# Kernel tuning notes

Measured on AMD Instinct MI355X. Metric: run time of the kernel, lower is better.

## Reference

```python
import jax, jax.numpy as jnp
import numpy as np

GAMMAS = jnp.array([2.0, 1.0, 0.5, 0.25, 0.125], dtype=jnp.float32)
K_NUM = 5
SIGN = 1.0  # min_distance=False


def setup_inputs() -> dict:
    key = jax.random.key(0)
    k1, k2 = jax.random.split(key)
    Xs = jax.random.normal(k1, (2048, 512), dtype=jnp.float32)
    Xt = jax.random.normal(k2, (2048, 512), dtype=jnp.float32)
    return {"Xs": Xs, "Xt": Xt}


def _rbf_multi(X1, X2):
    # pairwise squared distances [n1, n2], then K gamma bands -> [K, n1, n2]
    d = (X1 ** 2).sum(1)[:, None] + (X2 ** 2).sum(1)[None, :] - 2.0 * (X1 @ X2.T)
    return jnp.exp(-d[None, :, :] / (2.0 * GAMMAS[:, None, None] ** 2))


def _solve_simplex_qp(Q, p):
    # min 0.5 b^T Q b + p^T b  s.t. b >= 0, sum(b) = 1  (Q PD, K=5)
    # Exact global solve by enumerating all 31 nonempty active sets (KKT).
    K = Q.shape[0]
    masks = jnp.array([[(bits >> j) & 1 for j in range(K)]
                       for bits in range(1, 2 ** K)], dtype=Q.dtype)  # [31, K]

    def solve_one(m):
        M = jnp.zeros((K + 1, K + 1), Q.dtype)
        M = M.at[:K, :K].set(m[:, None] * Q * m[None, :] + jnp.diag(1.0 - m))
        M = M.at[:K, K].set(m)
        M = M.at[K, :K].set(m)
        rhs = jnp.concatenate([-m * p, jnp.ones((1,), Q.dtype)])
        sol = jnp.linalg.solve(M, rhs)
        beta = sol[:K] * m
        obj = 0.5 * beta @ Q @ beta + p @ beta
        feas = jnp.all(beta >= -1e-7)
        return beta, jnp.where(feas, obj, jnp.inf)

    betas, objs = jax.vmap(solve_one)(masks)
    return betas[jnp.argmin(objs)]


def reference(Xs, Xt):
    n = Xs.shape[0]
    XX = _rbf_multi(Xs, Xs)
    YY = _rbf_multi(Xt, Xt)
    YX = _rbf_multi(Xt, Xs)
    XY = _rbf_multi(Xs, Xt)
    g = XX + YY - XY - YX  # [K, n, n]

    # estimate_eta_k: pairs (i, i+1), i = 0,2,4,...
    i2 = jnp.arange(0, n, 2)
    h = g[:, i2, i2 + 1]  # [K, n/2]
    eta_p_k = 2.0 * h.sum(axis=1) / n  # [K]

    # estimate_qk_vector: h_d = h(i) - h(i+2), i = 0,4,8,...
    # inner double loop adds outer(h_d,h_d) with diagonal counted twice.
    h4 = h[:, 0::2] - h[:, 1::2]  # [K, n/4]
    Q_p_k = 4.0 / n * (h4 @ h4.T + jnp.diag((h4 ** 2).sum(axis=1)))  # [K, K]

    Q = 2.0 * Q_p_k + 1e-5 * jnp.eye(K_NUM, dtype=Q_p_k.dtype)
    p = -eta_p_k
    beta = SIGN * _solve_simplex_qp(Q, p)

    eta_k = g.mean(axis=(1, 2))  # compute_mmd
    # original detaches beta before the final dot product
    return eta_k @ jax.lax.stop_gradient(beta)
```

## Files before the change

kernel.cpp:

```cpp
#include <hip/hip_runtime.h>
#include <math.h>

#define NROWS 2048
#define DIMS  512
#define KG    5

__device__ __constant__ float c_invc[KG] = {0.125f, 0.5f, 2.0f, 8.0f, 32.0f};

typedef __attribute__((ext_vector_type(4))) int i32x4;
typedef __attribute__((ext_vector_type(8))) short bf16x8;

__device__ __forceinline__ void gload_lds16(const void* g, void* l) {
    __builtin_amdgcn_global_load_lds(
        (const __attribute__((address_space(1))) unsigned int*)g,
        (__attribute__((address_space(3))) unsigned int*)l, 16, 0, 0);
}

__device__ __forceinline__ unsigned long long pack8(const float4 v0, const float4 v1, float inv) {
    const float vv[8] = {v0.x, v0.y, v0.z, v0.w, v1.x, v1.y, v1.z, v1.w};
    unsigned long long pk = 0;
#pragma unroll
    for (int e = 0; e < 8; ++e) {
        int q = (int)rintf(vv[e] * inv);
        q = q > 127 ? 127 : (q < -127 ? -127 : q);
        pk |= (unsigned long long)((unsigned)q & 0xffu) << (8 * e);
    }
    return pk;
}

__global__ void prep_kernel(const float* __restrict__ Xs, const float* __restrict__ Xt,
                            signed char* __restrict__ Xsq, signed char* __restrict__ Xtq,
                            float* __restrict__ ns, float* __restrict__ nt,
                            float* __restrict__ sa, float* __restrict__ st,
                            float* __restrict__ h) {
    const int pairI = blockIdx.x * 4 + (threadIdx.x >> 6);
    const int lane = threadIdx.x & 63;
    const int i = 2 * pairI, j = i + 1;

    const float* psi = Xs + (size_t)i * DIMS + lane * 8;
    const float* psj = Xs + (size_t)j * DIMS + lane * 8;
    const float* pti = Xt + (size_t)i * DIMS + lane * 8;
    const float* ptj = Xt + (size_t)j * DIMS + lane * 8;
    const float4 a0 = *(const float4*)psi, a1 = *(const float4*)(psi + 4);
    const float4 b0 = *(const float4*)psj, b1 = *(const float4*)(psj + 4);
    const float4 c0 = *(const float4*)pti, c1 = *(const float4*)(pti + 4);
    const float4 d0 = *(const float4*)ptj, d1 = *(const float4*)(ptj + 4);

#define DOT8(u0, u1, v0, v1) (u0.x*v0.x + u0.y*v0.y + u0.z*v0.z + u0.w*v0.w + \
                              u1.x*v1.x + u1.y*v1.y + u1.z*v1.z + u1.w*v1.w)
#define MAX8(u0, u1) fmaxf(fmaxf(fmaxf(fabsf(u0.x), fabsf(u0.y)), fmaxf(fabsf(u0.z), fabsf(u0.w))), \
                           fmaxf(fmaxf(fabsf(u1.x), fabsf(u1.y)), fmaxf(fabsf(u1.z), fabsf(u1.w))))
    float r[8];
    r[0] = DOT8(a0, a1, a0, a1);
    r[1] = DOT8(b0, b1, b0, b1);
    r[2] = DOT8(c0, c1, c0, c1);
    r[3] = DOT8(d0, d1, d0, d1);
    r[4] = DOT8(a0, a1, b0, b1);
    r[5] = DOT8(c0, c1, d0, d1);
    r[6] = DOT8(a0, a1, d0, d1);
    r[7] = DOT8(c0, c1, b0, b1);
    float mx[4] = {MAX8(a0, a1), MAX8(b0, b1), MAX8(c0, c1), MAX8(d0, d1)};
#undef DOT8
#undef MAX8

#pragma unroll
    for (int v = 0; v < 4; ++v)
        for (int off = 32; off > 0; off >>= 1) mx[v] = fmaxf(mx[v], __shfl_xor(mx[v], off, 64));

    float inv[4], scl[4];
#pragma unroll
    for (int v = 0; v < 4; ++v) {
        scl[v] = mx[v] * (1.f / 127.f);
        inv[v] = mx[v] > 0.f ? 127.f / mx[v] : 0.f;
    }

    *(unsigned long long*)(Xsq + (size_t)i * DIMS + lane * 8) = pack8(a0, a1, inv[0]);
    *(unsigned long long*)(Xsq + (size_t)j * DIMS + lane * 8) = pack8(b0, b1, inv[1]);
    *(unsigned long long*)(Xtq + (size_t)i * DIMS + lane * 8) = pack8(c0, c1, inv[2]);
    *(unsigned long long*)(Xtq + (size_t)j * DIMS + lane * 8) = pack8(d0, d1, inv[3]);

#pragma unroll
    for (int v = 0; v < 8; ++v)
        for (int off = 32; off > 0; off >>= 1) r[v] += __shfl_down(r[v], off, 64);

    if (lane == 0) {
        ns[i] = r[0]; ns[j] = r[1]; nt[i] = r[2]; nt[j] = r[3];
        sa[i] = scl[0]; sa[j] = scl[1]; st[i] = scl[2]; st[j] = scl[3];
#pragma unroll
        for (int g = 0; g < KG; ++g) {
            const float ic = c_invc[g];
            h[g * 1024 + pairI] = __expf(-(r[0] + r[1] - 2.f * r[4]) * ic)
                                + __expf(-(r[2] + r[3] - 2.f * r[5]) * ic)
                                - __expf(-(r[0] + r[3] - 2.f * r[6]) * ic)
                                - __expf(-(r[2] + r[1] - 2.f * r[7]) * ic);
        }
    }
}

__global__ __launch_bounds__(256, 2) void gram_kernel(const signed char* __restrict__ Xsq,
                                                      const signed char* __restrict__ Xtq,
                                                      const float* __restrict__ ns,
                                                      const float* __restrict__ nt,
                                                      const float* __restrict__ sa,
                                                      const float* __restrict__ st,
                                                      float* __restrict__ partial) {
    const int pair = blockIdx.z;
    const int bx = blockIdx.x, by = blockIdx.y;
    const int bidx = pair * 256 + by * 16 + bx;
    const int tid = threadIdx.x;
    if (pair < 2 && bx < by) {
        if (tid < KG) partial[bidx * 8 + tid] = 0.f;
        return;
    }

    const signed char* A = (pair == 1) ? Xtq : Xsq;
    const signed char* B = (pair == 0) ? Xsq : Xtq;
    const float* na = (pair == 1) ? nt : ns;
    const float* nb = (pair == 0) ? ns : nt;
    const float* sca = (pair == 1) ? st : sa;
    const float* scb = (pair == 0) ? sa : st;
    const int row0 = by * 128, col0 = bx * 128;

    __shared__ signed char Asm[2][128 * 64];
    __shared__ signed char Bsm[2][128 * 64];

    const int lane = tid & 63;
    const int w = tid >> 6;
    const int wr = w >> 1, wc = w & 1;

    i32x4 acc[4][4] = {};

    const int srow = lane >> 2;
    const int schunk = lane & 3;

#define STAGE(buf, kt)                                                              \
    {                                                                               \
        _Pragma("unroll")                                                           \
        for (int q = 0; q < 2; ++q) {                                               \
            const int rbase = q * 64 + w * 16;                                      \
            const int rloc = rbase + srow;                                          \
            const int csrc = (schunk ^ ((rloc >> 1) & 3)) * 16;                     \
            gload_lds16(A + (size_t)(row0 + rloc) * DIMS + (kt) + csrc,             \
                        &Asm[buf][rbase * 64]);                                     \
            gload_lds16(B + (size_t)(col0 + rloc) * DIMS + (kt) + csrc,             \
                        &Bsm[buf][rbase * 64]);                                     \
        }                                                                           \
    }

    STAGE(0, 0);
    __syncthreads();

    const int rl = lane & 15, kq = lane >> 4;
#pragma unroll
    for (int t = 0; t < 8; ++t) {
        const int cur = t & 1;
        if (t < 7) STAGE(cur ^ 1, (t + 1) * 64);

        i32x4 af[4], bv[4];
#pragma unroll
        for (int m = 0; m < 4; ++m) {
            const int ra = wr * 64 + m * 16 + rl;
            af[m] = *(const i32x4*)&Asm[cur][ra * 64 + ((kq ^ ((ra >> 1) & 3)) * 16)];
            const int rb = wc * 64 + m * 16 + rl;
            bv[m] = *(const i32x4*)&Bsm[cur][rb * 64 + ((kq ^ ((rb >> 1) & 3)) * 16)];
        }
#pragma unroll
        for (int m = 0; m < 4; ++m)
#pragma unroll
            for (int n = 0; n < 4; ++n)
                acc[m][n] = __builtin_amdgcn_mfma_i32_16x16x64_i8(af[m], bv[n], acc[m][n], 0, 0, 0);
        __syncthreads();
    }
#undef STAGE

    float lsum[KG] = {0.f, 0.f, 0.f, 0.f, 0.f};
    const int gcol0 = col0 + wc * 64 + rl;
    const int grow0 = row0 + wr * 64 + kq * 4;
    const bool diagTile = (pair < 2) && (bx == by);
    const float wgt = (pair == 2) ? 1.f : 2.f;

    float colnorm[4], colscale[4];
#pragma unroll
    for (int n = 0; n < 4; ++n) {
        colnorm[n] = nb[gcol0 + n * 16];
        colscale[n] = scb[gcol0 + n * 16];
    }

#pragma unroll
    for (int m = 0; m < 4; ++m) {
        const float4 rn4 = *(const float4*)&na[grow0 + m * 16];
        const float4 rs4 = *(const float4*)&sca[grow0 + m * 16];
        const float rn[4] = {rn4.x, rn4.y, rn4.z, rn4.w};
        const float rs[4] = {rs4.x, rs4.y, rs4.z, rs4.w};
#pragma unroll
        for (int jj = 0; jj < 4; ++jj) {
            const int grow = grow0 + m * 16 + jj;
#pragma unroll
            for (int n = 0; n < 4; ++n) {
                const int gcol = gcol0 + n * 16;
                const float d = rn[jj] + colnorm[n]
                              - 2.f * (rs[jj] * colscale[n]) * (float)acc[m][n][jj];
                if (diagTile && gcol == grow) {
#pragma unroll
                    for (int g = 0; g < KG; ++g) lsum[g] += 1.f;
                } else if ((!diagTile || gcol > grow) && d < 840.f) {
                    float e = __expf(-d * 0.125f);
#pragma unroll
                    for (int g = 0; g < KG; ++g) {
                        lsum[g] += wgt * e;
                        const float e2 = e * e;
                        e = e2 * e2;
                    }
                }
            }
        }
    }

    __shared__ float redf[KG][4];
#pragma unroll
    for (int g = 0; g < KG; ++g) {
        float v = lsum[g];
        for (int off = 32; off > 0; off >>= 1) v += __shfl_down(v, off, 64);
        if (lane == 0) redf[g][w] = v;
    }
    __syncthreads();
    if (tid < KG)
        partial[bidx * 8 + tid] = redf[tid][0] + redf[tid][1] + redf[tid][2] + redf[tid][3];
}

__global__ void finalize_kernel(const float* __restrict__ partial,
                                const float* __restrict__ h,
                                float* __restrict__ out) {
    __shared__ float h4[KG][512];
    __shared__ float hsumS[KG];
    __shared__ float qdotS[15];
    __shared__ float redh[KG][4];
    __shared__ double sumsS[16];
    const int t = threadIdx.x;
    const int wv = t >> 6, ln = t & 63;

    if (wv < 3) {
        double s[KG] = {0.0, 0.0, 0.0, 0.0, 0.0};
        for (int b = ln; b < 256; b += 64) {
            const float* p = &partial[(wv * 256 + b) * 8];
#pragma unroll
            for (int g = 0; g < KG; ++g) s[g] += (double)p[g];
        }
#pragma unroll
        for (int g = 0; g < KG; ++g) {
            double v = s[g];
            for (int off = 32; off > 0; off >>= 1) v += __shfl_down(v, off, 64);
            if (ln == 0) sumsS[wv * KG + g] = v;
        }
    }

    for (int k = 0; k < KG; ++k)
        for (int j2 = t; j2 < 512; j2 += 256)
            h4[k][j2] = h[k * 1024 + 2 * j2] - h[k * 1024 + 2 * j2 + 1];

    {
        float s[KG] = {0.f, 0.f, 0.f, 0.f, 0.f};
        for (int j = t; j < 1024; j += 256)
#pragma unroll
            for (int k = 0; k < KG; ++k) s[k] += h[k * 1024 + j];
#pragma unroll
        for (int k = 0; k < KG; ++k) {
            float v = s[k];
            for (int off = 32; off > 0; off >>= 1) v += __shfl_down(v, off, 64);
            if (ln == 0) redh[k][wv] = v;
        }
    }
    __syncthreads();
    if (t < KG) hsumS[t] = redh[t][0] + redh[t][1] + redh[t][2] + redh[t][3];
    __syncthreads();

    const int pa[15] = {0,0,0,0,0,1,1,1,1,2,2,2,3,3,4};
    const int pb[15] = {0,1,2,3,4,1,2,3,4,2,3,4,3,4,4};
    for (int pi = wv; pi < 15; pi += 4) {
        float s = 0.f;
        for (int j = ln; j < 512; j += 64) s += h4[pa[pi]][j] * h4[pb[pi]][j];
        for (int off = 32; off > 0; off >>= 1) s += __shfl_down(s, off, 64);
        if (ln == 0) qdotS[pi] = s;
    }
    __syncthreads();

    if (t < 64) {
        const double n = 2048.0;
        double Q[KG][KG], p[KG], eta[KG];
        {
            int idx = 0;
            double dd[KG][KG];
#pragma unroll
            for (int a = 0; a < KG; ++a)
#pragma unroll
                for (int b = a; b < KG; ++b) { dd[a][b] = qdotS[idx]; dd[b][a] = qdotS[idx]; ++idx; }
#pragma unroll
            for (int a = 0; a < KG; ++a)
#pragma unroll
                for (int b = 0; b < KG; ++b) {
                    double qp = (4.0 / n) * (dd[a][b] + ((a == b) ? dd[a][a] : 0.0));
                    Q[a][b] = 2.0 * qp + ((a == b) ? 1e-5 : 0.0);
                }
        }
#pragma unroll
        for (int k = 0; k < KG; ++k) {
            p[k] = -2.0 * (double)hsumS[k] / n;
            eta[k] = (sumsS[k] + sumsS[KG + k] - 2.0 * sumsS[2 * KG + k]) / (n * n);
        }

        const int mask = t;
        const bool valid = (mask >= 1 && mask < 32);
        double beta[KG] = {0, 0, 0, 0, 0};
        double obj = INFINITY;

        if (valid) {
            double m[KG];
#pragma unroll
            for (int k = 0; k < KG; ++k) m[k] = (mask >> k) & 1 ? 1.0 : 0.0;
            double M[6][7];
#pragma unroll
            for (int a = 0; a < 6; ++a)
#pragma unroll
                for (int b = 0; b < 7; ++b) M[a][b] = 0.0;
#pragma unroll
            for (int a = 0; a < KG; ++a) {
#pragma unroll
                for (int b = 0; b < KG; ++b) M[a][b] = m[a] * Q[a][b] * m[b];
                M[a][a] += 1.0 - m[a];
                M[a][KG] = m[a];
                M[KG][a] = m[a];
                M[a][6] = -m[a] * p[a];
            }
            M[KG][6] = 1.0;
#pragma unroll
            for (int col = 0; col < 6; ++col) {
                const double dinv = 1.0 / M[col][col];
#pragma unroll
                for (int rr = 0; rr < 6; ++rr) {
                    if (rr > col) {
                        const double f = M[rr][col] * dinv;
#pragma unroll
                        for (int c = 0; c < 7; ++c)
                            if (c >= col) M[rr][c] -= f * M[col][c];
                    }
                }
            }
            double sol[6];
#pragma unroll
            for (int rr = 5; rr >= 0; --rr) {
                double s = M[rr][6];
#pragma unroll
                for (int c = 0; c < 6; ++c)
                    if (c > rr) s -= M[rr][c] * sol[c];
                sol[rr] = s / M[rr][rr];
            }
#pragma unroll
            for (int k = 0; k < KG; ++k) beta[k] = sol[k] * m[k];
            double o = 0.0;
#pragma unroll
            for (int a = 0; a < KG; ++a) {
                double qb = 0.0;
#pragma unroll
                for (int b = 0; b < KG; ++b) qb += Q[a][b] * beta[b];
                o += 0.5 * beta[a] * qb + p[a] * beta[a];
            }
            bool feas = true;
#pragma unroll
            for (int k = 0; k < KG; ++k) if (!(beta[k] >= -1e-7)) feas = false;
            obj = feas ? o : INFINITY;
        }

        double bobj = obj;
        int blane = valid ? mask : 9999;
        for (int off = 32; off > 0; off >>= 1) {
            const double o2 = __shfl_down(bobj, off, 64);
            const int l2 = __shfl_down(blane, off, 64);
            if (o2 < bobj || (o2 == bobj && l2 < blane)) { bobj = o2; blane = l2; }
        }
        bobj = __shfl(bobj, 0, 64);
        blane = __shfl(blane, 0, 64);
        if (bobj > 1e300) blane = 1;

        if (mask == blane) {
            double o = 0.0;
#pragma unroll
            for (int k = 0; k < KG; ++k) o += eta[k] * beta[k];
            out[0] = (float)o;
        }
    }
}

extern "C" void kernel_launch(void* const* d_in, const int* in_sizes, int n_in,
                              void* d_out, int out_size, void* d_ws, size_t ws_size,
                              hipStream_t stream) {
    const float* Xs = (const float*)d_in[0];
    const float* Xt = (const float*)d_in[1];
    float* out = (float*)d_out;

    char* ws = (char*)d_ws;
    float* partial = (float*)ws;
    float* ns = (float*)(ws + 24576);
    float* nt = (float*)(ws + 32768);
    float* sa = (float*)(ws + 40960);
    float* st = (float*)(ws + 49152);
    float* h  = (float*)(ws + 57344);
    signed char* Xsq = (signed char*)(ws + 131072);
    signed char* Xtq = (signed char*)(ws + 131072 + 1048576);

    prep_kernel<<<256, 256, 0, stream>>>(Xs, Xt, Xsq, Xtq, ns, nt, sa, st, h);
    gram_kernel<<<dim3(16, 16, 3), 256, 0, stream>>>(Xsq, Xtq, ns, nt, sa, st, partial);
    finalize_kernel<<<1, 256, 0, stream>>>(partial, h, out);
}
```

Before: 37.09 us.

## Treat stacked Xs/Xt as one Gram matrix and compute only upper-triangle tiles

The two inputs are quantized into one stacked 4096-row matrix, and the gram kernel launches only the 528 upper-triangle 128x128 tiles. Cross blocks get weight -2 and diagonal blocks are handled symmetrically. This removes the early-exit blocks of the old 768-block grid and the separate XY pass. The K step per stage is also doubled to 128 with a wider LDS swizzle, which halves the number of barriers but doubles LDS use per block. Tile decode uses a serial while loop per block.

```diff
diff --git a/kernel.cpp b/kernel.cpp
--- a/kernel.cpp
+++ b/kernel.cpp
@@ -2,13 +2,14 @@
 #include <math.h>
 
 #define NROWS 2048
+#define ZROWS 4096
 #define DIMS  512
 #define KG    5
+#define NJOBS 528
 
 __device__ __constant__ float c_invc[KG] = {0.125f, 0.5f, 2.0f, 8.0f, 32.0f};
 
 typedef __attribute__((ext_vector_type(4))) int i32x4;
-typedef __attribute__((ext_vector_type(8))) short bf16x8;
 
 __device__ __forceinline__ void gload_lds16(const void* g, void* l) {
     __builtin_amdgcn_global_load_lds(
@@ -29,9 +30,8 @@
 }
 
 __global__ void prep_kernel(const float* __restrict__ Xs, const float* __restrict__ Xt,
-                            signed char* __restrict__ Xsq, signed char* __restrict__ Xtq,
-                            float* __restrict__ ns, float* __restrict__ nt,
-                            float* __restrict__ sa, float* __restrict__ st,
+                            signed char* __restrict__ Zq,
+                            float* __restrict__ nz, float* __restrict__ sz,
                             float* __restrict__ h) {
     const int pairI = blockIdx.x * 4 + (threadIdx.x >> 6);
     const int lane = threadIdx.x & 63;
@@ -74,18 +74,18 @@
         inv[v] = mx[v] > 0.f ? 127.f / mx[v] : 0.f;
     }
 
-    *(unsigned long long*)(Xsq + (size_t)i * DIMS + lane * 8) = pack8(a0, a1, inv[0]);
-    *(unsigned long long*)(Xsq + (size_t)j * DIMS + lane * 8) = pack8(b0, b1, inv[1]);
-    *(unsigned long long*)(Xtq + (size_t)i * DIMS + lane * 8) = pack8(c0, c1, inv[2]);
-    *(unsigned long long*)(Xtq + (size_t)j * DIMS + lane * 8) = pack8(d0, d1, inv[3]);
+    *(unsigned long long*)(Zq + (size_t)i * DIMS + lane * 8)            = pack8(a0, a1, inv[0]);
+    *(unsigned long long*)(Zq + (size_t)j * DIMS + lane * 8)            = pack8(b0, b1, inv[1]);
+    *(unsigned long long*)(Zq + (size_t)(NROWS + i) * DIMS + lane * 8)  = pack8(c0, c1, inv[2]);
+    *(unsigned long long*)(Zq + (size_t)(NROWS + j) * DIMS + lane * 8)  = pack8(d0, d1, inv[3]);
 
 #pragma unroll
     for (int v = 0; v < 8; ++v)
         for (int off = 32; off > 0; off >>= 1) r[v] += __shfl_down(r[v], off, 64);
 
     if (lane == 0) {
-        ns[i] = r[0]; ns[j] = r[1]; nt[i] = r[2]; nt[j] = r[3];
-        sa[i] = scl[0]; sa[j] = scl[1]; st[i] = scl[2]; st[j] = scl[3];
+        nz[i] = r[0]; nz[j] = r[1]; nz[NROWS + i] = r[2]; nz[NROWS + j] = r[3];
+        sz[i] = scl[0]; sz[j] = scl[1]; sz[NROWS + i] = scl[2]; sz[NROWS + j] = scl[3];
 #pragma unroll
         for (int g = 0; g < KG; ++g) {
             const float ic = c_invc[g];
@@ -97,53 +97,39 @@
     }
 }
 
-__global__ __launch_bounds__(256, 2) void gram_kernel(const signed char* __restrict__ Xsq,
-                                                      const signed char* __restrict__ Xtq,
-                                                      const float* __restrict__ ns,
-                                                      const float* __restrict__ nt,
-                                                      const float* __restrict__ sa,
-                                                      const float* __restrict__ st,
+__global__ __launch_bounds__(256, 2) void gram_kernel(const signed char* __restrict__ Zq,
+                                                      const float* __restrict__ nz,
+                                                      const float* __restrict__ sz,
                                                       float* __restrict__ partial) {
-    const int pair = blockIdx.z;
-    const int bx = blockIdx.x, by = blockIdx.y;
-    const int bidx = pair * 256 + by * 16 + bx;
+    int job = blockIdx.x;
+    int by = 0;
+    while (job >= (32 - by)) { job -= (32 - by); ++by; }
+    const int bx = by + job;
+
+    const int row0 = by * 128, col0 = bx * 128;
     const int tid = threadIdx.x;
-    if (pair < 2 && bx < by) {
-        if (tid < KG) partial[bidx * 8 + tid] = 0.f;
-        return;
-    }
-
-    const signed char* A = (pair == 1) ? Xtq : Xsq;
-    const signed char* B = (pair == 0) ? Xsq : Xtq;
-    const float* na = (pair == 1) ? nt : ns;
-    const float* nb = (pair == 0) ? ns : nt;
-    const float* sca = (pair == 1) ? st : sa;
-    const float* scb = (pair == 0) ? sa : st;
-    const int row0 = by * 128, col0 = bx * 128;
-
-    __shared__ signed char Asm[2][128 * 64];
-    __shared__ signed char Bsm[2][128 * 64];
-
     const int lane = tid & 63;
     const int w = tid >> 6;
     const int wr = w >> 1, wc = w & 1;
 
+    __shared__ signed char Asm[2][128 * 128];
+    __shared__ signed char Bsm[2][128 * 128];
+
     i32x4 acc[4][4] = {};
 
-    const int srow = lane >> 2;
-    const int schunk = lane & 3;
+    const int lrow = lane >> 3;
+    const int lchunk = (lane & 7) ^ lrow;
 
 #define STAGE(buf, kt)                                                              \
     {                                                                               \
         _Pragma("unroll")                                                           \
-        for (int q = 0; q < 2; ++q) {                                               \
-            const int rbase = q * 64 + w * 16;                                      \
-            const int rloc = rbase + srow;                                          \
-            const int csrc = (schunk ^ ((rloc >> 1) & 3)) * 16;                     \
-            gload_lds16(A + (size_t)(row0 + rloc) * DIMS + (kt) + csrc,             \
-                        &Asm[buf][rbase * 64]);                                     \
-            gload_lds16(B + (size_t)(col0 + rloc) * DIMS + (kt) + csrc,             \
-                        &Bsm[buf][rbase * 64]);                                     \
+        for (int q = 0; q < 4; ++q) {                                               \
+            const int rbase = w * 32 + q * 8;                                       \
+            const int rloc = rbase + lrow;                                          \
+            gload_lds16(Zq + (size_t)(row0 + rloc) * DIMS + (kt) + lchunk * 16,     \
+                        &Asm[buf][rbase * 128]);                                    \
+            gload_lds16(Zq + (size_t)(col0 + rloc) * DIMS + (kt) + lchunk * 16,     \
+                        &Bsm[buf][rbase * 128]);                                    \
         }                                                                           \
     }
 
@@ -152,23 +138,26 @@
 
     const int rl = lane & 15, kq = lane >> 4;
 #pragma unroll
-    for (int t = 0; t < 8; ++t) {
+    for (int t = 0; t < 4; ++t) {
         const int cur = t & 1;
-        if (t < 7) STAGE(cur ^ 1, (t + 1) * 64);
-
-        i32x4 af[4], bv[4];
-#pragma unroll
-        for (int m = 0; m < 4; ++m) {
-            const int ra = wr * 64 + m * 16 + rl;
-            af[m] = *(const i32x4*)&Asm[cur][ra * 64 + ((kq ^ ((ra >> 1) & 3)) * 16)];
-            const int rb = wc * 64 + m * 16 + rl;
-            bv[m] = *(const i32x4*)&Bsm[cur][rb * 64 + ((kq ^ ((rb >> 1) & 3)) * 16)];
-        }
-#pragma unroll
-        for (int m = 0; m < 4; ++m)
-#pragma unroll
-            for (int n = 0; n < 4; ++n)
-                acc[m][n] = __builtin_amdgcn_mfma_i32_16x16x64_i8(af[m], bv[n], acc[m][n], 0, 0, 0);
+        if (t < 3) STAGE(cur ^ 1, (t + 1) * 128);
+
+#pragma unroll
+        for (int sub = 0; sub < 2; ++sub) {
+            i32x4 af[4], bv[4];
+#pragma unroll
+            for (int m = 0; m < 4; ++m) {
+                const int ra = wr * 64 + m * 16 + rl;
+                af[m] = *(const i32x4*)&Asm[cur][ra * 128 + (((sub * 4 + kq) ^ (ra & 7)) * 16)];
+                const int rb = wc * 64 + m * 16 + rl;
+                bv[m] = *(const i32x4*)&Bsm[cur][rb * 128 + (((sub * 4 + kq) ^ (rb & 7)) * 16)];
+            }
+#pragma unroll
+            for (int m = 0; m < 4; ++m)
+#pragma unroll
+                for (int n = 0; n < 4; ++n)
+                    acc[m][n] = __builtin_amdgcn_mfma_i32_16x16x64_i8(af[m], bv[n], acc[m][n], 0, 0, 0);
+        }
         __syncthreads();
     }
 #undef STAGE
@@ -176,20 +165,21 @@
     float lsum[KG] = {0.f, 0.f, 0.f, 0.f, 0.f};
     const int gcol0 = col0 + wc * 64 + rl;
     const int grow0 = row0 + wr * 64 + kq * 4;
-    const bool diagTile = (pair < 2) && (bx == by);
-    const float wgt = (pair == 2) ? 1.f : 2.f;
+    const bool diagTile = (bx == by);
+    const bool sameQuad = ((bx < 16) == (by < 16));
+    const float wgt = sameQuad ? 2.f : -2.f;
 
     float colnorm[4], colscale[4];
 #pragma unroll
     for (int n = 0; n < 4; ++n) {
-        colnorm[n] = nb[gcol0 + n * 16];
-        colscale[n] = scb[gcol0 + n * 16];
+        colnorm[n] = nz[gcol0 + n * 16];
+        colscale[n] = sz[gcol0 + n * 16];
     }
 
 #pragma unroll
     for (int m = 0; m < 4; ++m) {
-        const float4 rn4 = *(const float4*)&na[grow0 + m * 16];
-        const float4 rs4 = *(const float4*)&sca[grow0 + m * 16];
+        const float4 rn4 = *(const float4*)&nz[grow0 + m * 16];
+        const float4 rs4 = *(const float4*)&sz[grow0 + m * 16];
         const float rn[4] = {rn4.x, rn4.y, rn4.z, rn4.w};
         const float rs[4] = {rs4.x, rs4.y, rs4.z, rs4.w};
 #pragma unroll
@@ -225,7 +215,7 @@
     }
     __syncthreads();
     if (tid < KG)
-        partial[bidx * 8 + tid] = redf[tid][0] + redf[tid][1] + redf[tid][2] + redf[tid][3];
+        partial[blockIdx.x * 8 + tid] = redf[tid][0] + redf[tid][1] + redf[tid][2] + redf[tid][3];
 }
 
 __global__ void finalize_kernel(const float* __restrict__ partial,
@@ -235,14 +225,15 @@
     __shared__ float hsumS[KG];
     __shared__ float qdotS[15];
     __shared__ float redh[KG][4];
-    __shared__ double sumsS[16];
+    __shared__ double redd[4][KG];
+    __shared__ double sumsS[KG];
     const int t = threadIdx.x;
     const int wv = t >> 6, ln = t & 63;
 
-    if (wv < 3) {
+    {
         double s[KG] = {0.0, 0.0, 0.0, 0.0, 0.0};
-        for (int b = ln; b < 256; b += 64) {
-            const float* p = &partial[(wv * 256 + b) * 8];
+        for (int b = t; b < NJOBS; b += 256) {
+            const float* p = &partial[b * 8];
 #pragma unroll
             for (int g = 0; g < KG; ++g) s[g] += (double)p[g];
         }
@@ -250,7 +241,7 @@
         for (int g = 0; g < KG; ++g) {
             double v = s[g];
             for (int off = 32; off > 0; off >>= 1) v += __shfl_down(v, off, 64);
-            if (ln == 0) sumsS[wv * KG + g] = v;
+            if (ln == 0) redd[wv][g] = v;
         }
     }
 
@@ -271,7 +262,10 @@
         }
     }
     __syncthreads();
-    if (t < KG) hsumS[t] = redh[t][0] + redh[t][1] + redh[t][2] + redh[t][3];
+    if (t < KG) {
+        hsumS[t] = redh[t][0] + redh[t][1] + redh[t][2] + redh[t][3];
+        sumsS[t] = redd[0][t] + redd[1][t] + redd[2][t] + redd[3][t];
+    }
     __syncthreads();
 
     const int pa[15] = {0,0,0,0,0,1,1,1,1,2,2,2,3,3,4};
@@ -305,7 +299,7 @@
 #pragma unroll
         for (int k = 0; k < KG; ++k) {
             p[k] = -2.0 * (double)hsumS[k] / n;
-            eta[k] = (sumsS[k] + sumsS[KG + k] - 2.0 * sumsS[2 * KG + k]) / (n * n);
+            eta[k] = sumsS[k] / (n * n);
         }
 
         const int mask = t;
@@ -399,15 +393,12 @@
 
     char* ws = (char*)d_ws;
     float* partial = (float*)ws;
-    float* ns = (float*)(ws + 24576);
-    float* nt = (float*)(ws + 32768);
-    float* sa = (float*)(ws + 40960);
-    float* st = (float*)(ws + 49152);
-    float* h  = (float*)(ws + 57344);
-    signed char* Xsq = (signed char*)(ws + 131072);
-    signed char* Xtq = (signed char*)(ws + 131072 + 1048576);
-
-    prep_kernel<<<256, 256, 0, stream>>>(Xs, Xt, Xsq, Xtq, ns, nt, sa, st, h);
-    gram_kernel<<<dim3(16, 16, 3), 256, 0, stream>>>(Xsq, Xtq, ns, nt, sa, st, partial);
+    float* nz = (float*)(ws + 32768);
+    float* sz = (float*)(ws + 32768 + 16384);
+    float* h  = (float*)(ws + 65536);
+    signed char* Zq = (signed char*)(ws + 131072);
+
+    prep_kernel<<<256, 256, 0, stream>>>(Xs, Xt, Zq, nz, sz, h);
+    gram_kernel<<<NJOBS, 256, 0, stream>>>(Zq, nz, sz, partial);
     finalize_kernel<<<1, 256, 0, stream>>>(partial, h, out);
 }
```

After: 42.61 us. 14.9% more time.

## Split single-block finalize into parallel reduce kernel and tiny QP kernel

Applied to the files above, without the earlier changes.

Replaces the single-block finalize kernel with a 25-block reduce kernel and a separate 64-thread QP-solve kernel. Each reduce block computes one Q dot product, one h sum or one weighted eta sum. The partial buffer is transposed to a gamma-major layout so those loads are coalesced. The aim is to spread the serial reduction work across many CUs, at the cost of one extra kernel launch.

```diff
diff --git a/kernel.cpp b/kernel.cpp
--- a/kernel.cpp
+++ b/kernel.cpp
@@ -8,7 +8,6 @@
 __device__ __constant__ float c_invc[KG] = {0.125f, 0.5f, 2.0f, 8.0f, 32.0f};
 
 typedef __attribute__((ext_vector_type(4))) int i32x4;
-typedef __attribute__((ext_vector_type(8))) short bf16x8;
 
 __device__ __forceinline__ void gload_lds16(const void* g, void* l) {
     __builtin_amdgcn_global_load_lds(
@@ -109,7 +108,7 @@
     const int bidx = pair * 256 + by * 16 + bx;
     const int tid = threadIdx.x;
     if (pair < 2 && bx < by) {
-        if (tid < KG) partial[bidx * 8 + tid] = 0.f;
+        if (tid < KG) partial[tid * 768 + bidx] = 0.f;
         return;
     }
 
@@ -225,168 +224,147 @@
     }
     __syncthreads();
     if (tid < KG)
-        partial[bidx * 8 + tid] = redf[tid][0] + redf[tid][1] + redf[tid][2] + redf[tid][3];
-}
-
-__global__ void finalize_kernel(const float* __restrict__ partial,
-                                const float* __restrict__ h,
-                                float* __restrict__ out) {
-    __shared__ float h4[KG][512];
-    __shared__ float hsumS[KG];
-    __shared__ float qdotS[15];
-    __shared__ float redh[KG][4];
-    __shared__ double sumsS[16];
+        partial[tid * 768 + bidx] = redf[tid][0] + redf[tid][1] + redf[tid][2] + redf[tid][3];
+}
+
+__global__ void reduce_kernel(const float* __restrict__ partial,
+                              const float* __restrict__ h,
+                              double* __restrict__ qhr) {
+    const int bid = blockIdx.x;
     const int t = threadIdx.x;
-    const int wv = t >> 6, ln = t & 63;
-
-    if (wv < 3) {
-        double s[KG] = {0.0, 0.0, 0.0, 0.0, 0.0};
-        for (int b = ln; b < 256; b += 64) {
-            const float* p = &partial[(wv * 256 + b) * 8];
-#pragma unroll
-            for (int g = 0; g < KG; ++g) s[g] += (double)p[g];
-        }
-#pragma unroll
-        for (int g = 0; g < KG; ++g) {
-            double v = s[g];
-            for (int off = 32; off > 0; off >>= 1) v += __shfl_down(v, off, 64);
-            if (ln == 0) sumsS[wv * KG + g] = v;
-        }
-    }
-
-    for (int k = 0; k < KG; ++k)
-        for (int j2 = t; j2 < 512; j2 += 256)
-            h4[k][j2] = h[k * 1024 + 2 * j2] - h[k * 1024 + 2 * j2 + 1];
-
+    __shared__ double red[4];
+
+    double s = 0.0;
+    if (bid < 15) {
+        const int pa[15] = {0,0,0,0,0,1,1,1,1,2,2,2,3,3,4};
+        const int pb[15] = {0,1,2,3,4,1,2,3,4,2,3,4,3,4,4};
+        const float* ha = h + pa[bid] * 1024;
+        const float* hb = h + pb[bid] * 1024;
+        for (int j = t; j < 512; j += 256) {
+            const float va = ha[2 * j] - ha[2 * j + 1];
+            const float vb = hb[2 * j] - hb[2 * j + 1];
+            s += (double)(va * vb);
+        }
+    } else if (bid < 20) {
+        const float* hg = h + (bid - 15) * 1024;
+        for (int j = t; j < 1024; j += 256) s += (double)hg[j];
+    } else {
+        const int g = bid - 20;
+        for (int b = t; b < 768; b += 256) {
+            const float wv = (b >> 8) == 2 ? -2.f : 1.f;
+            s += (double)(wv * partial[g * 768 + b]);
+        }
+    }
+
+    for (int off = 32; off > 0; off >>= 1) s += __shfl_down(s, off, 64);
+    if ((t & 63) == 0) red[t >> 6] = s;
+    __syncthreads();
+    if (t == 0) qhr[bid] = red[0] + red[1] + red[2] + red[3];
+}
+
+__global__ void qp_kernel(const double* __restrict__ qhr, float* __restrict__ out) {
+    const int t = threadIdx.x;
+    const double n = 2048.0;
+    double Q[KG][KG], p[KG], eta[KG];
     {
-        float s[KG] = {0.f, 0.f, 0.f, 0.f, 0.f};
-        for (int j = t; j < 1024; j += 256)
-#pragma unroll
-            for (int k = 0; k < KG; ++k) s[k] += h[k * 1024 + j];
-#pragma unroll
-        for (int k = 0; k < KG; ++k) {
-            float v = s[k];
-            for (int off = 32; off > 0; off >>= 1) v += __shfl_down(v, off, 64);
-            if (ln == 0) redh[k][wv] = v;
-        }
-    }
-    __syncthreads();
-    if (t < KG) hsumS[t] = redh[t][0] + redh[t][1] + redh[t][2] + redh[t][3];
-    __syncthreads();
-
-    const int pa[15] = {0,0,0,0,0,1,1,1,1,2,2,2,3,3,4};
-    const int pb[15] = {0,1,2,3,4,1,2,3,4,2,3,4,3,4,4};
-    for (int pi = wv; pi < 15; pi += 4) {
-        float s = 0.f;
-        for (int j = ln; j < 512; j += 64) s += h4[pa[pi]][j] * h4[pb[pi]][j];
-        for (int off = 32; off > 0; off >>= 1) s += __shfl_down(s, off, 64);
-        if (ln == 0) qdotS[pi] = s;
-    }
-    __syncthreads();
-
-    if (t < 64) {
-        const double n = 2048.0;
-        double Q[KG][KG], p[KG], eta[KG];
-        {
-            int idx = 0;
-            double dd[KG][KG];
-#pragma unroll
-            for (int a = 0; a < KG; ++a)
-#pragma unroll
-                for (int b = a; b < KG; ++b) { dd[a][b] = qdotS[idx]; dd[b][a] = qdotS[idx]; ++idx; }
-#pragma unroll
-            for (int a = 0; a < KG; ++a)
-#pragma unroll
-                for (int b = 0; b < KG; ++b) {
-                    double qp = (4.0 / n) * (dd[a][b] + ((a == b) ? dd[a][a] : 0.0));
-                    Q[a][b] = 2.0 * qp + ((a == b) ? 1e-5 : 0.0);
-                }
-        }
-#pragma unroll
-        for (int k = 0; k < KG; ++k) {
-            p[k] = -2.0 * (double)hsumS[k] / n;
-            eta[k] = (sumsS[k] + sumsS[KG + k] - 2.0 * sumsS[2 * KG + k]) / (n * n);
-        }
-
-        const int mask = t;
-        const bool valid = (mask >= 1 && mask < 32);
-        double beta[KG] = {0, 0, 0, 0, 0};
-        double obj = INFINITY;
-
-        if (valid) {
-            double m[KG];
-#pragma unroll
-            for (int k = 0; k < KG; ++k) m[k] = (mask >> k) & 1 ? 1.0 : 0.0;
-            double M[6][7];
-#pragma unroll
-            for (int a = 0; a < 6; ++a)
-#pragma unroll
-                for (int b = 0; b < 7; ++b) M[a][b] = 0.0;
-#pragma unroll
-            for (int a = 0; a < KG; ++a) {
-#pragma unroll
-                for (int b = 0; b < KG; ++b) M[a][b] = m[a] * Q[a][b] * m[b];
-                M[a][a] += 1.0 - m[a];
-                M[a][KG] = m[a];
-                M[KG][a] = m[a];
-                M[a][6] = -m[a] * p[a];
+        int idx = 0;
+        double dd[KG][KG];
+#pragma unroll
+        for (int a = 0; a < KG; ++a)
+#pragma unroll
+            for (int b = a; b < KG; ++b) { dd[a][b] = qhr[idx]; dd[b][a] = qhr[idx]; ++idx; }
+#pragma unroll
+        for (int a = 0; a < KG; ++a)
+#pragma unroll
+            for (int b = 0; b < KG; ++b) {
+                double qp = (4.0 / n) * (dd[a][b] + ((a == b) ? dd[a][a] : 0.0));
+                Q[a][b] = 2.0 * qp + ((a == b) ? 1e-5 : 0.0);
             }
-            M[KG][6] = 1.0;
-#pragma unroll
-            for (int col = 0; col < 6; ++col) {
-                const double dinv = 1.0 / M[col][col];
-#pragma unroll
-                for (int rr = 0; rr < 6; ++rr) {
-                    if (rr > col) {
-                        const double f = M[rr][col] * dinv;
-#pragma unroll
-                        for (int c = 0; c < 7; ++c)
-                            if (c >= col) M[rr][c] -= f * M[col][c];
-                    }
+    }
+#pragma unroll
+    for (int k = 0; k < KG; ++k) {
+        p[k] = -2.0 * qhr[15 + k] / n;
+        eta[k] = qhr[20 + k] / (n * n);
+    }
+
+    const int mask = t;
+    const bool valid = (mask >= 1 && mask < 32);
+    double beta[KG] = {0, 0, 0, 0, 0};
+    double obj = INFINITY;
+
+    if (valid) {
+        double m[KG];
+#pragma unroll
+        for (int k = 0; k < KG; ++k) m[k] = (mask >> k) & 1 ? 1.0 : 0.0;
+        double M[6][7];
+#pragma unroll
+        for (int a = 0; a < 6; ++a)
+#pragma unroll
+            for (int b = 0; b < 7; ++b) M[a][b] = 0.0;
+#pragma unroll
+        for (int a = 0; a < KG; ++a) {
+#pragma unroll
+            for (int b = 0; b < KG; ++b) M[a][b] = m[a] * Q[a][b] * m[b];
+            M[a][a] += 1.0 - m[a];
+            M[a][KG] = m[a];
+            M[KG][a] = m[a];
+            M[a][6] = -m[a] * p[a];
+        }
+        M[KG][6] = 1.0;
+#pragma unroll
+        for (int col = 0; col < 6; ++col) {
+            const double dinv = 1.0 / M[col][col];
+#pragma unroll
+            for (int rr = 0; rr < 6; ++rr) {
+                if (rr > col) {
+                    const double f = M[rr][col] * dinv;
+#pragma unroll
+                    for (int c = 0; c < 7; ++c)
+                        if (c >= col) M[rr][c] -= f * M[col][c];
                 }
             }
-            double sol[6];
-#pragma unroll
-            for (int rr = 5; rr >= 0; --rr) {
-                double s = M[rr][6];
-#pragma unroll
-                for (int c = 0; c < 6; ++c)
-                    if (c > rr) s -= M[rr][c] * sol[c];
-                sol[rr] = s / M[rr][rr];
-            }
-#pragma unroll
-            for (int k = 0; k < KG; ++k) beta[k] = sol[k] * m[k];
-            double o = 0.0;
-#pragma unroll
-            for (int a = 0; a < KG; ++a) {
-                double qb = 0.0;
-#pragma unroll
-                for (int b = 0; b < KG; ++b) qb += Q[a][b] * beta[b];
-                o += 0.5 * beta[a] * qb + p[a] * beta[a];
-            }
-            bool feas = true;
-#pragma unroll
-            for (int k = 0; k < KG; ++k) if (!(beta[k] >= -1e-7)) feas = false;
-            obj = feas ? o : INFINITY;
-        }
-
-        double bobj = obj;
-        int blane = valid ? mask : 9999;
-        for (int off = 32; off > 0; off >>= 1) {
-            const double o2 = __shfl_down(bobj, off, 64);
-            const int l2 = __shfl_down(blane, off, 64);
-            if (o2 < bobj || (o2 == bobj && l2 < blane)) { bobj = o2; blane = l2; }
-        }
-        bobj = __shfl(bobj, 0, 64);
-        blane = __shfl(blane, 0, 64);
-        if (bobj > 1e300) blane = 1;
-
-        if (mask == blane) {
-            double o = 0.0;
-#pragma unroll
-            for (int k = 0; k < KG; ++k) o += eta[k] * beta[k];
-            out[0] = (float)o;
-        }
+        }
+        double sol[6];
+#pragma unroll
+        for (int rr = 5; rr >= 0; --rr) {
+            double s = M[rr][6];
+#pragma unroll
+            for (int c = 0; c < 6; ++c)
+                if (c > rr) s -= M[rr][c] * sol[c];
+            sol[rr] = s / M[rr][rr];
+        }
+#pragma unroll
+        for (int k = 0; k < KG; ++k) beta[k] = sol[k] * m[k];
+        double o = 0.0;
+#pragma unroll
+        for (int a = 0; a < KG; ++a) {
+            double qb = 0.0;
+#pragma unroll
+            for (int b = 0; b < KG; ++b) qb += Q[a][b] * beta[b];
+            o += 0.5 * beta[a] * qb + p[a] * beta[a];
+        }
+        bool feas = true;
+#pragma unroll
+        for (int k = 0; k < KG; ++k) if (!(beta[k] >= -1e-7)) feas = false;
+        obj = feas ? o : INFINITY;
+    }
+
+    double bobj = obj;
+    int blane = valid ? mask : 9999;
+    for (int off = 32; off > 0; off >>= 1) {
+        const double o2 = __shfl_down(bobj, off, 64);
+        const int l2 = __shfl_down(blane, off, 64);
+        if (o2 < bobj || (o2 == bobj && l2 < blane)) { bobj = o2; blane = l2; }
+    }
+    bobj = __shfl(bobj, 0, 64);
+    blane = __shfl(blane, 0, 64);
+    if (bobj > 1e300) blane = 1;
+
+    if (mask == blane) {
+        double o = 0.0;
+#pragma unroll
+        for (int k = 0; k < KG; ++k) o += eta[k] * beta[k];
+        out[0] = (float)o;
     }
 }
 
@@ -399,15 +377,17 @@
 
     char* ws = (char*)d_ws;
     float* partial = (float*)ws;
-    float* ns = (float*)(ws + 24576);
-    float* nt = (float*)(ws + 32768);
-    float* sa = (float*)(ws + 40960);
-    float* st = (float*)(ws + 49152);
-    float* h  = (float*)(ws + 57344);
+    float* ns = (float*)(ws + 16384);
+    float* nt = (float*)(ws + 24576);
+    float* sa = (float*)(ws + 32768);
+    float* st = (float*)(ws + 40960);
+    float* h  = (float*)(ws + 49152);
+    double* qhr = (double*)(ws + 98304);
     signed char* Xsq = (signed char*)(ws + 131072);
     signed char* Xtq = (signed char*)(ws + 131072 + 1048576);
 
     prep_kernel<<<256, 256, 0, stream>>>(Xs, Xt, Xsq, Xtq, ns, nt, sa, st, h);
     gram_kernel<<<dim3(16, 16, 3), 256, 0, stream>>>(Xsq, Xtq, ns, nt, sa, st, partial);
-    finalize_kernel<<<1, 256, 0, stream>>>(partial, h, out);
-}
+    reduce_kernel<<<25, 256, 0, stream>>>(partial, h, qhr);
+    qp_kernel<<<1, 64, 0, stream>>>(qhr, out);
+}
```

New measurement: 31.03 us, median of 2. 16.3% less time.
